# Performance work log

Hardware: AMD Instinct MI355X
Metric: run time of the kernel (lower is better)

The kernel has to match this reference:

```python
import jax, jax.numpy as jnp
import numpy as np

N = 204800  # total nodes in the batched graph
B = 4096    # number of graphs (sessions)
D = 128     # embedding_dim


def setup_inputs() -> dict:
    key = jax.random.key(0)
    ks = jax.random.split(key, 10)
    feat_i = jax.random.normal(ks[0], (N, D), dtype=jnp.float32)
    U_feat = jax.random.normal(ks[1], (B, D), dtype=jnp.float32)
    # per-node click counts >= 1 so log(cnt) is finite
    cnt = jax.random.uniform(ks[2], (N,), dtype=jnp.float32, minval=1.0, maxval=50.0)
    scale = 1.0 / np.sqrt(D)
    W_key = jax.random.normal(ks[3], (D, D), dtype=jnp.float32) * scale
    W_user = jax.random.normal(ks[4], (D, D), dtype=jnp.float32) * scale
    b_user = jax.random.normal(ks[5], (D,), dtype=jnp.float32) * scale
    W_last = jax.random.normal(ks[6], (D, D), dtype=jnp.float32) * scale
    w_e = jax.random.normal(ks[7], (D, 1), dtype=jnp.float32) * scale
    last_nodes = jax.random.randint(ks[8], (B,), 0, N, dtype=jnp.int32)
    segment_ids = jnp.sort(jax.random.randint(ks[9], (N,), 0, B, dtype=jnp.int32))
    return {
        "feat_i": feat_i, "U_feat": U_feat, "cnt": cnt,
        "W_key": W_key, "W_user": W_user, "b_user": b_user,
        "W_last": W_last, "w_e": w_e,
        "last_nodes": last_nodes, "segment_ids": segment_ids,
    }


def reference(feat_i, U_feat, cnt, W_key, W_user, b_user, W_last, w_e,
              last_nodes, segment_ids):
    # linear projections (torch Linear y = x W^T + b; weights here are stored
    # pre-transposed so x @ W is the same math)
    feat_key = feat_i @ W_key                       # [N, D]
    U = U_feat @ W_user + b_user                    # [B, D]
    last_feat = feat_i[last_nodes] @ W_last         # [B, D]
    # dgl.broadcast_nodes: per-graph query replicated onto its nodes
    feat_qry = (U + last_feat)[segment_ids]         # [N, D]
    # additive-sigmoid attention score + log-count bias
    e = jax.nn.sigmoid(feat_qry + feat_key) @ w_e   # [N, 1]
    e = e + jnp.log(cnt)[:, None]                   # [N, 1]
    # segment softmax over ragged per-graph node segments
    m = jax.ops.segment_max(e, segment_ids, num_segments=B)      # [B, 1]
    ex = jnp.exp(e - m[segment_ids])                             # [N, 1]
    s = jax.ops.segment_sum(ex, segment_ids, num_segments=B)     # [B, 1]
    alpha = ex / s[segment_ids]                                  # [N, 1]
    # weighted segment reduce over raw node features (feat_val = feat_i)
    rst = jax.ops.segment_sum(alpha * feat_i, segment_ids, num_segments=B)  # [B, D]
    return rst
```

## Files before the change

kernel.cpp:

```cpp
#include <hip/hip_runtime.h>
#include <hip/hip_bf16.h>
#include <math.h>

#define N_NODES 204800
#define B_GRAPHS 4096
#define DIM 128

typedef __attribute__((ext_vector_type(8))) short bf16x8;
typedef __attribute__((ext_vector_type(4))) float f32x4;

__device__ __forceinline__ float sigf(float x) {
    return 1.0f / (1.0f + __expf(-x));
}

__device__ __forceinline__ unsigned short bfrne(float x) {
    unsigned u = __float_as_uint(x);
    unsigned r = u + 0x7FFFu + ((u >> 16) & 1u);
    return (unsigned short)(r >> 16);
}

__global__ __launch_bounds__(128) void qkernel(
    const float* __restrict__ feat, const float* __restrict__ U_feat,
    const float* __restrict__ W_user, const float* __restrict__ b_user,
    const float* __restrict__ W_last, const int* __restrict__ last_nodes,
    const float* __restrict__ W_key, unsigned short* __restrict__ Wt,
    const int* __restrict__ seg, int* __restrict__ bounds,
    float* __restrict__ q) {
  if (blockIdx.x >= 576) {
    int n = (blockIdx.x - 576) * 128 + threadIdx.x;
    int sc = seg[n];
    int sp = (n == 0) ? -1 : seg[n - 1];
    for (int b = sp + 1; b <= sc; ++b) bounds[b] = (b == 0) ? 0 : n;
    if (n == N_NODES - 1)
      for (int b = sc + 1; b <= B_GRAPHS; ++b) bounds[b] = N_NODES;
    return;
  }
  if (blockIdx.x >= 512) {
    int b = blockIdx.x - 512;
#pragma unroll
    for (int j = 0; j < 2; ++j) {
      int o = b * 256 + j * 128 + threadIdx.x;
      int c = o >> 7, k = o & 127;
      Wt[o] = bfrne(W_key[k * DIM + c]);
    }
    return;
  }
  __shared__ float sU[8][DIM];
  __shared__ float sL[8][DIM];
  const int d = threadIdx.x;
  const int g0 = blockIdx.x * 8;
  for (int g = 0; g < 8; ++g) {
    sU[g][d] = U_feat[(g0 + g) * DIM + d];
    int ln = last_nodes[g0 + g];
    sL[g][d] = feat[ln * DIM + d];
  }
  __syncthreads();
  float acc[8];
#pragma unroll
  for (int g = 0; g < 8; ++g) acc[g] = 0.0f;

  for (int kk = 0; kk < 32; ++kk) {
    float wu[4], wl[4];
#pragma unroll
    for (int j = 0; j < 4; ++j) {
      wu[j] = W_user[(kk * 4 + j) * DIM + d];
      wl[j] = W_last[(kk * 4 + j) * DIM + d];
    }
#pragma unroll
    for (int g = 0; g < 8; ++g) {
      float4 u4 = reinterpret_cast<const float4*>(sU[g])[kk];
      float4 l4 = reinterpret_cast<const float4*>(sL[g])[kk];
      acc[g] += u4.x * wu[0] + u4.y * wu[1] + u4.z * wu[2] + u4.w * wu[3];
      acc[g] += l4.x * wl[0] + l4.y * wl[1] + l4.z * wl[2] + l4.w * wl[3];
    }
  }
  float bu = b_user[d];
  for (int g = 0; g < 8; ++g) q[(g0 + g) * DIM + d] = acc[g] + bu;
}

__global__ __launch_bounds__(512, 4) void ekernel(
    const float* __restrict__ feat, const unsigned short* __restrict__ Wt,
    const float* __restrict__ w_e, const float* __restrict__ cnt,
    const int* __restrict__ seg, const float* __restrict__ q,
    float* __restrict__ e) {
  __shared__ unsigned short sW[128 * DIM];
  __shared__ float sWe[DIM];
  const int tid = threadIdx.x;
  const int base = blockIdx.x * 128;
  const int l = tid & 63, w = tid >> 6;
  const int lr = l & 15, lh = l >> 4;
  const int node = base + w * 16 + lr;

  const int sg = seg[node];
  const float lc = cnt[node];

  const float* rp = feat + (size_t)node * DIM + lh * 8;
  float4 fv[4][2];
#pragma unroll
  for (int ks = 0; ks < 4; ++ks) {
    fv[ks][0] = *reinterpret_cast<const float4*>(rp + ks * 32);
    fv[ks][1] = *reinterpret_cast<const float4*>(rp + ks * 32 + 4);
  }

  const float4* q4p = reinterpret_cast<const float4*>(q);
  float4 qv[8];
#pragma unroll
  for (int c = 0; c < 8; ++c) qv[c] = q4p[(size_t)sg * 32 + c * 4 + lh];

  const uint4* Wt4 = reinterpret_cast<const uint4*>(Wt);
#pragma unroll
  for (int i = 0; i < 4; ++i) {
    int hw = i * 4096 + tid * 8;
    int row = hw >> 7, k0 = hw & 127;
    uint4 wv = Wt4[i * 512 + tid];
    *reinterpret_cast<uint4*>(&sW[row * DIM + (k0 ^ ((row & 7) << 3))]) = wv;
  }
  if (tid < 32)
    reinterpret_cast<float4*>(sWe)[tid] =
        reinterpret_cast<const float4*>(w_e)[tid];

  bf16x8 af[4];
#pragma unroll
  for (int ks = 0; ks < 4; ++ks) {
    union { bf16x8 v; unsigned short u[8]; } a;
    a.u[0] = bfrne(fv[ks][0].x); a.u[1] = bfrne(fv[ks][0].y);
    a.u[2] = bfrne(fv[ks][0].z); a.u[3] = bfrne(fv[ks][0].w);
    a.u[4] = bfrne(fv[ks][1].x); a.u[5] = bfrne(fv[ks][1].y);
    a.u[6] = bfrne(fv[ks][1].z); a.u[7] = bfrne(fv[ks][1].w);
    af[ks] = a.v;
  }

  __syncthreads();

  float p = 0.0f;
#pragma unroll
  for (int c = 0; c < 8; ++c) {
    const int row = c * 16 + lr;
    bf16x8 wf[4];
#pragma unroll
    for (int ks = 0; ks < 4; ++ks)
      wf[ks] = *reinterpret_cast<const bf16x8*>(
          &sW[row * DIM + ((ks * 32 + lh * 8) ^ ((row & 7) << 3))]);
    float4 we = *reinterpret_cast<const float4*>(&sWe[c * 16 + lh * 4]);

    f32x4 a0 = f32x4{0.f, 0.f, 0.f, 0.f};
#pragma unroll
    for (int ks = 0; ks < 4; ++ks)
      a0 = __builtin_amdgcn_mfma_f32_16x16x32_bf16(wf[ks], af[ks], a0, 0, 0, 0);

    float4 qc = qv[c];
    p += we.x * sigf(a0[0] + qc.x) + we.y * sigf(a0[1] + qc.y) +
         we.z * sigf(a0[2] + qc.z) + we.w * sigf(a0[3] + qc.w);
  }

  p += __shfl_xor(p, 16, 64);
  p += __shfl_xor(p, 32, 64);
  if (lh == 0) e[node] = p + __logf(lc);
}

__global__ __launch_bounds__(256) void skernel(
    const float* __restrict__ feat, const int* __restrict__ bounds,
    float* __restrict__ e, float* __restrict__ rst) {
  const int b = blockIdx.x;
  const int tid = threadIdx.x;
  const int s0 = bounds[b];
  const int s1 = bounds[b + 1];

  if (s1 <= s0) {
    if (tid < DIM) rst[b * DIM + tid] = 0.0f;
    return;
  }

  __shared__ float red[8];
  __shared__ float part[8 * DIM];
  const int wave = tid >> 6, lane = tid & 63;

  float lm = -3.0e38f;
  for (int i = s0 + tid; i < s1; i += 256) lm = fmaxf(lm, e[i]);
#pragma unroll
  for (int off = 32; off >= 1; off >>= 1) lm = fmaxf(lm, __shfl_xor(lm, off, 64));
  if (lane == 0) red[wave] = lm;
  __syncthreads();
  const float m = fmaxf(fmaxf(red[0], red[1]), fmaxf(red[2], red[3]));

  float ls = 0.0f;
  for (int i = s0 + tid; i < s1; i += 256) {
    float p = __expf(e[i] - m);
    e[i] = p;
    ls += p;
  }
#pragma unroll
  for (int off = 32; off >= 1; off >>= 1) ls += __shfl_xor(ls, off, 64);
  if (lane == 0) red[4 + wave] = ls;
  __syncthreads();
  const float inv = 1.0f / (red[4] + red[5] + red[6] + red[7]);

  const int c = tid & 31;
  const int h = tid >> 5;
  float4 acc = float4{0.f, 0.f, 0.f, 0.f};
  const float4* feat4 = reinterpret_cast<const float4*>(feat);
  for (int n = s0 + h; n < s1; n += 8) {
    float p = e[n];
    float4 f = feat4[n * 32 + c];
    acc.x += p * f.x;
    acc.y += p * f.y;
    acc.z += p * f.z;
    acc.w += p * f.w;
  }
  reinterpret_cast<float4*>(part)[h * 32 + c] = acc;
  __syncthreads();
  if (tid < DIM) {
    float tot = 0.0f;
#pragma unroll
    for (int hh = 0; hh < 8; ++hh) tot += part[hh * DIM + tid];
    rst[b * DIM + tid] = tot * inv;
  }
}

extern "C" void kernel_launch(void* const* d_in, const int* in_sizes, int n_in,
                              void* d_out, int out_size, void* d_ws,
                              size_t ws_size, hipStream_t stream) {
  const float* feat = (const float*)d_in[0];
  const float* U_feat = (const float*)d_in[1];
  const float* cnt = (const float*)d_in[2];
  const float* W_key = (const float*)d_in[3];
  const float* W_user = (const float*)d_in[4];
  const float* b_user = (const float*)d_in[5];
  const float* W_last = (const float*)d_in[6];
  const float* w_e = (const float*)d_in[7];
  const int* last_nodes = (const int*)d_in[8];
  const int* seg = (const int*)d_in[9];
  float* out = (float*)d_out;

  float* q = (float*)d_ws;
  float* e = q + B_GRAPHS * DIM;
  unsigned short* Wt = (unsigned short*)(e + N_NODES);
  int* bounds = (int*)(Wt + DIM * DIM);

  qkernel<<<512 + 64 + N_NODES / 128, 128, 0, stream>>>(
      feat, U_feat, W_user, b_user, W_last, last_nodes, W_key, Wt, seg, bounds, q);
  ekernel<<<N_NODES / 128, 512, 0, stream>>>(feat, Wt, w_e, cnt, seg, q, e);
  skernel<<<B_GRAPHS, 256, 0, stream>>>(feat, bounds, e, out);
}
```

Before: 63.78 us.

## Fuse score and segment-softmax kernels into one per-graph kernel

Merges the per-node attention-score kernel and the per-segment softmax/reduce kernel into one kernel launched per graph. Scores are kept in shared memory instead of a global e buffer, and each block reads its node features twice, with the second read likely hitting cache. W_key fragments are now loaded straight from global memory rather than staged in swizzled LDS. The cost is load imbalance from ragged segment lengths, repeated global fetches of the weight tile per 64-node chunk, and a fixed SE_CAP of 1024 that gives wrong results for segments longer than that.

```diff
diff --git a/kernel.cpp b/kernel.cpp
--- a/kernel.cpp
+++ b/kernel.cpp
@@ -5,6 +5,7 @@
 #define N_NODES 204800
 #define B_GRAPHS 4096
 #define DIM 128
+#define SE_CAP 1024
 
 typedef __attribute__((ext_vector_type(8))) short bf16x8;
 typedef __attribute__((ext_vector_type(4))) float f32x4;
@@ -78,105 +79,86 @@
   for (int g = 0; g < 8; ++g) q[(g0 + g) * DIM + d] = acc[g] + bu;
 }
 
-__global__ __launch_bounds__(512, 4) void ekernel(
+__global__ __launch_bounds__(256, 4) void gkernel(
     const float* __restrict__ feat, const unsigned short* __restrict__ Wt,
     const float* __restrict__ w_e, const float* __restrict__ cnt,
-    const int* __restrict__ seg, const float* __restrict__ q,
-    float* __restrict__ e) {
-  __shared__ unsigned short sW[128 * DIM];
-  __shared__ float sWe[DIM];
+    const int* __restrict__ bounds, const float* __restrict__ q,
+    float* __restrict__ rst) {
+  const int b = blockIdx.x;
   const int tid = threadIdx.x;
-  const int base = blockIdx.x * 128;
+  const int s0 = bounds[b], s1 = bounds[b + 1];
+  const int len = s1 - s0;
+  if (len <= 0) {
+    if (tid < DIM) rst[b * DIM + tid] = 0.0f;
+    return;
+  }
+
+  __shared__ float se[SE_CAP];
+  __shared__ float sQ[DIM];
+  __shared__ float red[8];
+  __shared__ float part[8 * DIM];
+
+  if (tid < 32)
+    reinterpret_cast<float4*>(sQ)[tid] =
+        reinterpret_cast<const float4*>(q)[(size_t)b * 32 + tid];
+  __syncthreads();
+
   const int l = tid & 63, w = tid >> 6;
   const int lr = l & 15, lh = l >> 4;
-  const int node = base + w * 16 + lr;
-
-  const int sg = seg[node];
-  const float lc = cnt[node];
-
-  const float* rp = feat + (size_t)node * DIM + lh * 8;
-  float4 fv[4][2];
-#pragma unroll
-  for (int ks = 0; ks < 4; ++ks) {
-    fv[ks][0] = *reinterpret_cast<const float4*>(rp + ks * 32);
-    fv[ks][1] = *reinterpret_cast<const float4*>(rp + ks * 32 + 4);
-  }
-
-  const float4* q4p = reinterpret_cast<const float4*>(q);
-  float4 qv[8];
-#pragma unroll
-  for (int c = 0; c < 8; ++c) qv[c] = q4p[(size_t)sg * 32 + c * 4 + lh];
-
-  const uint4* Wt4 = reinterpret_cast<const uint4*>(Wt);
-#pragma unroll
-  for (int i = 0; i < 4; ++i) {
-    int hw = i * 4096 + tid * 8;
-    int row = hw >> 7, k0 = hw & 127;
-    uint4 wv = Wt4[i * 512 + tid];
-    *reinterpret_cast<uint4*>(&sW[row * DIM + (k0 ^ ((row & 7) << 3))]) = wv;
-  }
-  if (tid < 32)
-    reinterpret_cast<float4*>(sWe)[tid] =
-        reinterpret_cast<const float4*>(w_e)[tid];
-
-  bf16x8 af[4];
-#pragma unroll
-  for (int ks = 0; ks < 4; ++ks) {
-    union { bf16x8 v; unsigned short u[8]; } a;
-    a.u[0] = bfrne(fv[ks][0].x); a.u[1] = bfrne(fv[ks][0].y);
-    a.u[2] = bfrne(fv[ks][0].z); a.u[3] = bfrne(fv[ks][0].w);
-    a.u[4] = bfrne(fv[ks][1].x); a.u[5] = bfrne(fv[ks][1].y);
-    a.u[6] = bfrne(fv[ks][1].z); a.u[7] = bfrne(fv[ks][1].w);
-    af[ks] = a.v;
-  }
-
-  __syncthreads();
-
-  float p = 0.0f;
-#pragma unroll
-  for (int c = 0; c < 8; ++c) {
-    const int row = c * 16 + lr;
-    bf16x8 wf[4];
-#pragma unroll
-    for (int ks = 0; ks < 4; ++ks)
-      wf[ks] = *reinterpret_cast<const bf16x8*>(
-          &sW[row * DIM + ((ks * 32 + lh * 8) ^ ((row & 7) << 3))]);
-    float4 we = *reinterpret_cast<const float4*>(&sWe[c * 16 + lh * 4]);
-
-    f32x4 a0 = f32x4{0.f, 0.f, 0.f, 0.f};
-#pragma unroll
-    for (int ks = 0; ks < 4; ++ks)
-      a0 = __builtin_amdgcn_mfma_f32_16x16x32_bf16(wf[ks], af[ks], a0, 0, 0, 0);
-
-    float4 qc = qv[c];
-    p += we.x * sigf(a0[0] + qc.x) + we.y * sigf(a0[1] + qc.y) +
-         we.z * sigf(a0[2] + qc.z) + we.w * sigf(a0[3] + qc.w);
-  }
-
-  p += __shfl_xor(p, 16, 64);
-  p += __shfl_xor(p, 32, 64);
-  if (lh == 0) e[node] = p + __logf(lc);
-}
-
-__global__ __launch_bounds__(256) void skernel(
-    const float* __restrict__ feat, const int* __restrict__ bounds,
-    float* __restrict__ e, float* __restrict__ rst) {
-  const int b = blockIdx.x;
-  const int tid = threadIdx.x;
-  const int s0 = bounds[b];
-  const int s1 = bounds[b + 1];
-
-  if (s1 <= s0) {
-    if (tid < DIM) rst[b * DIM + tid] = 0.0f;
-    return;
-  }
-
-  __shared__ float red[8];
-  __shared__ float part[8 * DIM];
+
+  for (int start = s0; start < s1; start += 64) {
+    const int ni = start + w * 16 + lr;
+    const int nc = (ni < s1) ? ni : (s1 - 1);
+
+    const float* rp = feat + (size_t)nc * DIM + lh * 8;
+    float4 fv[4][2];
+#pragma unroll
+    for (int ks = 0; ks < 4; ++ks) {
+      fv[ks][0] = *reinterpret_cast<const float4*>(rp + ks * 32);
+      fv[ks][1] = *reinterpret_cast<const float4*>(rp + ks * 32 + 4);
+    }
+    bf16x8 af[4];
+#pragma unroll
+    for (int ks = 0; ks < 4; ++ks) {
+      union { bf16x8 v; unsigned short u[8]; } a;
+      a.u[0] = bfrne(fv[ks][0].x); a.u[1] = bfrne(fv[ks][0].y);
+      a.u[2] = bfrne(fv[ks][0].z); a.u[3] = bfrne(fv[ks][0].w);
+      a.u[4] = bfrne(fv[ks][1].x); a.u[5] = bfrne(fv[ks][1].y);
+      a.u[6] = bfrne(fv[ks][1].z); a.u[7] = bfrne(fv[ks][1].w);
+      af[ks] = a.v;
+    }
+
+    float p = 0.0f;
+#pragma unroll
+    for (int c = 0; c < 8; ++c) {
+      bf16x8 wf[4];
+#pragma unroll
+      for (int ks = 0; ks < 4; ++ks)
+        wf[ks] = *reinterpret_cast<const bf16x8*>(
+            &Wt[(c * 16 + lr) * DIM + ks * 32 + lh * 8]);
+
+      f32x4 a0 = f32x4{0.f, 0.f, 0.f, 0.f};
+#pragma unroll
+      for (int ks = 0; ks < 4; ++ks)
+        a0 = __builtin_amdgcn_mfma_f32_16x16x32_bf16(wf[ks], af[ks], a0, 0, 0, 0);
+
+      float4 we = *reinterpret_cast<const float4*>(&w_e[c * 16 + lh * 4]);
+      float4 qc = *reinterpret_cast<const float4*>(&sQ[c * 16 + lh * 4]);
+      p += we.x * sigf(a0[0] + qc.x) + we.y * sigf(a0[1] + qc.y) +
+           we.z * sigf(a0[2] + qc.z) + we.w * sigf(a0[3] + qc.w);
+    }
+    p += __shfl_xor(p, 16, 64);
+    p += __shfl_xor(p, 32, 64);
+    if (lh == 0 && ni < s1 && (ni - s0) < SE_CAP)
+      se[ni - s0] = p + __logf(cnt[ni]);
+  }
+  __syncthreads();
+
+  const int lcap = (len < SE_CAP) ? len : SE_CAP;
   const int wave = tid >> 6, lane = tid & 63;
 
   float lm = -3.0e38f;
-  for (int i = s0 + tid; i < s1; i += 256) lm = fmaxf(lm, e[i]);
+  for (int i = tid; i < lcap; i += 256) lm = fmaxf(lm, se[i]);
 #pragma unroll
   for (int off = 32; off >= 1; off >>= 1) lm = fmaxf(lm, __shfl_xor(lm, off, 64));
   if (lane == 0) red[wave] = lm;
@@ -184,10 +166,10 @@
   const float m = fmaxf(fmaxf(red[0], red[1]), fmaxf(red[2], red[3]));
 
   float ls = 0.0f;
-  for (int i = s0 + tid; i < s1; i += 256) {
-    float p = __expf(e[i] - m);
-    e[i] = p;
-    ls += p;
+  for (int i = tid; i < lcap; i += 256) {
+    float pp = __expf(se[i] - m);
+    se[i] = pp;
+    ls += pp;
   }
 #pragma unroll
   for (int off = 32; off >= 1; off >>= 1) ls += __shfl_xor(ls, off, 64);
@@ -195,19 +177,19 @@
   __syncthreads();
   const float inv = 1.0f / (red[4] + red[5] + red[6] + red[7]);
 
-  const int c = tid & 31;
+  const int c2 = tid & 31;
   const int h = tid >> 5;
   float4 acc = float4{0.f, 0.f, 0.f, 0.f};
   const float4* feat4 = reinterpret_cast<const float4*>(feat);
   for (int n = s0 + h; n < s1; n += 8) {
-    float p = e[n];
-    float4 f = feat4[n * 32 + c];
-    acc.x += p * f.x;
-    acc.y += p * f.y;
-    acc.z += p * f.z;
-    acc.w += p * f.w;
-  }
-  reinterpret_cast<float4*>(part)[h * 32 + c] = acc;
+    float pp = se[(n - s0) < SE_CAP ? (n - s0) : (SE_CAP - 1)];
+    float4 f = feat4[(size_t)n * 32 + c2];
+    acc.x += pp * f.x;
+    acc.y += pp * f.y;
+    acc.z += pp * f.z;
+    acc.w += pp * f.w;
+  }
+  reinterpret_cast<float4*>(part)[h * 32 + c2] = acc;
   __syncthreads();
   if (tid < DIM) {
     float tot = 0.0f;
@@ -233,12 +215,10 @@
   float* out = (float*)d_out;
 
   float* q = (float*)d_ws;
-  float* e = q + B_GRAPHS * DIM;
-  unsigned short* Wt = (unsigned short*)(e + N_NODES);
+  unsigned short* Wt = (unsigned short*)(q + B_GRAPHS * DIM);
   int* bounds = (int*)(Wt + DIM * DIM);
 
   qkernel<<<512 + 64 + N_NODES / 128, 128, 0, stream>>>(
       feat, U_feat, W_user, b_user, W_last, last_nodes, W_key, Wt, seg, bounds, q);
-  ekernel<<<N_NODES / 128, 512, 0, stream>>>(feat, Wt, w_e, cnt, seg, q, e);
-  skernel<<<B_GRAPHS, 256, 0, stream>>>(feat, bounds, e, out);
-}
+  gkernel<<<B_GRAPHS, 256, 0, stream>>>(feat, Wt, w_e, cnt, bounds, q, out);
+}
```

New measurement: 219.0 us. 243% more time.
